# Performance work log

Measured on AMD Instinct MI355X. Metric: run time of the kernel, lower is better.

## Reference

```python
import jax, jax.numpy as jnp
import numpy as np
import itertools

# ---- static configuration (matches init_kwargs) ----
LS = [0, 1, 2, 3]            # spherical harmonic degrees, parity (-1)^l
MUL = 128                    # channel multiplicity of hklm / output
N_EDGES = 16384
DIMS = [2 * l + 1 for l in LS]
Y_DIM = sum(DIMS)                        # 16
H_DIM = sum(d * MUL for d in DIMS)       # 2048
Y_OFF = np.cumsum([0] + DIMS).tolist()
H_OFF = np.cumsum([0] + [d * MUL for d in DIMS]).tolist()

# ---- real-basis O(3) Clebsch-Gordan coefficients (numpy, setup-time) ----
def _su2_generators(l):
    m = np.arange(-l, l + 1)
    Lz = np.diag(m).astype(np.complex128)
    vals = np.sqrt(l * (l + 1) - m[:-1] * (m[:-1] + 1))
    Lp = np.zeros((2 * l + 1, 2 * l + 1), np.complex128)
    Lp[np.arange(1, 2 * l + 1), np.arange(2 * l)] = vals
    Lm = Lp.T.copy()
    return (Lp + Lm) / 2.0, (Lp - Lm) / 2.0j, Lz

def _c2r(l):
    # unitary change of basis: complex SH -> real SH
    d = 2 * l + 1
    U = np.zeros((d, d), np.complex128)
    U[l, l] = 1.0
    s2 = 1.0 / np.sqrt(2.0)
    for m in range(1, l + 1):
        U[l + m, l + m] = (-1) ** m * s2
        U[l + m, l - m] = s2
        U[l - m, l + m] = -1j * (-1) ** m * s2
        U[l - m, l - m] = 1j * s2
    return U

def _real_generators(l):
    U = _c2r(l)
    return [np.real(-1j * (U @ L @ U.conj().T)) for L in _su2_generators(l)]

def _cg(l1, l2, l3):
    # invariant tensor = null space of the summed infinitesimal rotation action
    G1, G2, G3 = _real_generators(l1), _real_generators(l2), _real_generators(l3)
    d1, d2, d3 = 2 * l1 + 1, 2 * l2 + 1, 2 * l3 + 1
    I1, I2, I3 = np.eye(d1), np.eye(d2), np.eye(d3)
    rows = []
    for k in range(3):
        rows.append(np.kron(np.kron(G1[k], I2), I3)
                    + np.kron(np.kron(I1, G2[k]), I3)
                    + np.kron(np.kron(I1, I2), G3[k]))
    K = np.concatenate(rows, axis=0)
    _, s, Vt = np.linalg.svd(K)
    c = Vt[-1].reshape(d1, d2, d3)
    c = c / np.linalg.norm(c)
    c = c * np.sign(c.reshape(-1)[np.argmax(np.abs(c))])  # deterministic sign
    return c

PATHS = []
_CG_LIST = []
for (i1, l1), (i2, l2), (i3, l3) in itertools.product(enumerate(LS), enumerate(LS), enumerate(LS)):
    # triangle inequality + O3 parity selection rule ((-1)^l parities)
    if abs(l1 - l2) <= l3 <= l1 + l2 and (l1 + l2 + l3) % 2 == 0:
        PATHS.append((i1, i2, i3))
        _CG_LIST.append(_cg(l1, l2, l3))
N_PATHS = len(PATHS)                    # 23
W_DIM = N_PATHS * MUL                   # 2944
CG_OFF = np.cumsum([0] + [c.size for c in _CG_LIST]).tolist()
CGC_NP = np.concatenate([c.reshape(-1) for c in _CG_LIST]).astype(np.float32)


def setup_inputs() -> dict:
    key = jax.random.key(0)
    k1, k2, k3 = jax.random.split(key, 3)
    return {
        "Ylm": jax.random.normal(k1, (N_EDGES, Y_DIM), jnp.float32),
        "hklm": jax.random.normal(k2, (N_EDGES, H_DIM), jnp.float32),
        "weight": jax.random.normal(k3, (N_EDGES, W_DIM), jnp.float32),
        "CGC": jnp.asarray(CGC_NP),   # registered buffer in the torch module
    }


def reference(Ylm, hklm, weight, CGC):
    # segmented tensor product 'abcu,a,bu,cu' with per-path weight fused in:
    # out[n, c, u] += sum_{a,b} CG_p[a,b,c] * w_p[n,u] * Y[n,a] * h[n,b,u]
    N = Ylm.shape[0]
    out = jnp.zeros((N, H_DIM), Ylm.dtype)
    for p, (i1, i2, i3) in enumerate(PATHS):
        d1, d2, d3 = DIMS[i1], DIMS[i2], DIMS[i3]
        cg = CGC[CG_OFF[p]:CG_OFF[p + 1]].reshape(d1, d2, d3)
        y = Ylm[:, Y_OFF[i1]:Y_OFF[i1] + d1]
        h = hklm[:, H_OFF[i2]:H_OFF[i2] + d2 * MUL].reshape(N, d2, MUL)
        w = weight[:, p * MUL:(p + 1) * MUL]
        z = jnp.einsum('abc,na,nbu->ncu', cg, y, h) * w[:, None, :]
        out = out.at[:, H_OFF[i3]:H_OFF[i3] + d3 * MUL].add(z.reshape(N, d3 * MUL))
    return out
```

## Files before the change

### kernel.cpp

```cpp
#include <hip/hip_runtime.h>


#define BS 256
#define GSZ 32
#define EPB 8
#define YD 16
#define HD 2048
#define WD 2944
#define NROW 99

#define FOR_PATHS(X) \
  X(0, 0,0,0,    0,  0) \
  X(1, 0,1,1,    1,  1) \
  X(2, 0,2,2,   10,  4) \
  X(3, 0,3,3,   35,  9) \
  X(4, 1,0,1,   84, 16) \
  X(5, 1,1,0,   93, 19) \
  X(6, 1,1,2,  102, 20) \
  X(7, 1,2,1,  147, 25) \
  X(8, 1,2,3,  192, 28) \
  X(9, 1,3,2,  297, 35) \
  X(10,2,0,2,  402, 40) \
  X(11,2,1,1,  427, 45) \
  X(12,2,1,3,  472, 48) \
  X(13,2,2,0,  577, 55) \
  X(14,2,2,2,  602, 56) \
  X(15,2,3,1,  727, 61) \
  X(16,2,3,3,  832, 64) \
  X(17,3,0,3, 1077, 71) \
  X(18,3,1,2, 1126, 78) \
  X(19,3,2,1, 1231, 83) \
  X(20,3,2,3, 1336, 86) \
  X(21,3,3,0, 1581, 93) \
  X(22,3,3,2, 1630, 94)

__host__ __device__ constexpr int coff(int l) {
  return l == 0 ? 0 : (l == 1 ? 1 : (l == 2 ? 4 : 9));
}

__global__ __launch_bounds__(BS, 2) void etp_kernel(
    const float* __restrict__ Y, const float* __restrict__ H,
    const float* __restrict__ W, const float* __restrict__ CG,
    float* __restrict__ O) {
  const int g = threadIdx.x >> 5;
  const int l = threadIdx.x & 31;
  const int n = blockIdx.x * EPB + g;

  __shared__ __align__(16) float Bsm[EPB][NROW * 8];
  __shared__ float ysm[EPB][YD];

  { const int t = threadIdx.x;
    if (t < EPB * YD) {
      const int e = t >> 4, c = t & 15;
      ysm[e][c] = Y[(size_t)(blockIdx.x * EPB + e) * YD + c];
    } }
  __syncthreads();

#define BUILD(P, L1, L2, L3, CGO, RO) { \
    constexpr int d1 = 2*(L1)+1, d2 = 2*(L2)+1, d3 = 2*(L3)+1; \
    _Pragma("unroll") \
    for (int it = 0; it < (d2 * d3 + GSZ - 1) / GSZ; ++it) { \
      const int idx = l + it * GSZ; \
      if (idx < d2 * d3) { \
        const int m3 = idx / d2, m2 = idx - m3 * d2; \
        float s = 0.f; \
        _Pragma("unroll") \
        for (int a = 0; a < d1; ++a) \
          s += CG[(CGO) + (a * d2 + m2) * d3 + m3] * ysm[g][coff(L1) + a]; \
        Bsm[g][((RO) + m3) * 8 + m2] = s; \
      } } }
  FOR_PATHS(BUILD)
#undef BUILD
  __syncthreads();

  const float4* __restrict__ Hp = (const float4*)(H + (size_t)n * HD);
  const float4* __restrict__ Wp = (const float4*)(W + (size_t)n * WD);
  float4* __restrict__ Op = (float4*)(O + (size_t)n * HD);

  float4 h[YD];
#pragma unroll
  for (int c = 0; c < YD; ++c) h[c] = Hp[c * GSZ + l];
#pragma unroll
  for (int c = 0; c < YD; ++c)
    asm volatile("" : "+v"(h[c].x), "+v"(h[c].y), "+v"(h[c].z), "+v"(h[c].w));

  float4 acc[YD];
#pragma unroll
  for (int c = 0; c < YD; ++c) acc[c] = make_float4(0.f, 0.f, 0.f, 0.f);

#define DOPATH(P, L1, L2, L3, CGO, RO) { \
    constexpr int d2 = 2*(L2)+1, d3 = 2*(L3)+1; \
    const float4 wv = Wp[(P) * GSZ + l]; \
    _Pragma("unroll") \
    for (int m3 = 0; m3 < d3; ++m3) { \
      const float4* row = (const float4*)&Bsm[g][((RO) + m3) * 8]; \
      float br[8]; \
      *(float4*)&br[0] = row[0]; \
      if (d2 > 4) *(float4*)&br[4] = row[1]; \
      float4 s = make_float4(0.f, 0.f, 0.f, 0.f); \
      _Pragma("unroll") \
      for (int m2 = 0; m2 < d2; ++m2) { \
        const float b = br[m2]; \
        const float4 hv = h[coff(L2) + m2]; \
        s.x += b * hv.x; s.y += b * hv.y; s.z += b * hv.z; s.w += b * hv.w; \
      } \
      float4& A = acc[coff(L3) + m3]; \
      A.x += s.x * wv.x; A.y += s.y * wv.y; A.z += s.z * wv.z; A.w += s.w * wv.w; \
    } }
  FOR_PATHS(DOPATH)
#undef DOPATH

#pragma unroll
  for (int c = 0; c < YD; ++c) Op[c * GSZ + l] = acc[c];
}

extern "C" void kernel_launch(void* const* d_in, const int* in_sizes, int n_in,
                              void* d_out, int out_size, void* d_ws, size_t ws_size,
                              hipStream_t stream) {
  const float* Y  = (const float*)d_in[0];
  const float* H  = (const float*)d_in[1];
  const float* W  = (const float*)d_in[2];
  const float* CG = (const float*)d_in[3];
  float* O = (float*)d_out;

  const int n_edges = in_sizes[0] / YD;
  etp_kernel<<<n_edges / EPB, BS, 0, stream>>>(Y, H, W, CG, O);
}
```

Baseline: 115.0 us.

## Preload all path weights, use ext_vector float4 math, nontemporal output stores

```diff
diff --git a/kernel.cpp b/kernel.cpp
--- a/kernel.cpp
+++ b/kernel.cpp
@@ -7,7 +7,10 @@
 #define YD 16
 #define HD 2048
 #define WD 2944
+#define NP 23
 #define NROW 99
+
+typedef float f4 __attribute__((ext_vector_type(4)));
 
 #define FOR_PATHS(X) \
   X(0, 0,0,0,    0,  0) \
@@ -38,7 +41,9 @@
   return l == 0 ? 0 : (l == 1 ? 1 : (l == 2 ? 4 : 9));
 }
 
-__global__ __launch_bounds__(BS, 2) void etp_kernel(
+__global__ __launch_bounds__(BS)
+__attribute__((amdgpu_waves_per_eu(2, 2)))
+void etp_kernel(
     const float* __restrict__ Y, const float* __restrict__ H,
     const float* __restrict__ W, const float* __restrict__ CG,
     float* __restrict__ O) {
@@ -73,45 +78,41 @@
 #undef BUILD
   __syncthreads();
 
-  const float4* __restrict__ Hp = (const float4*)(H + (size_t)n * HD);
-  const float4* __restrict__ Wp = (const float4*)(W + (size_t)n * WD);
-  float4* __restrict__ Op = (float4*)(O + (size_t)n * HD);
+  const f4* __restrict__ Hp = (const f4*)(H + (size_t)n * HD);
+  const f4* __restrict__ Wp = (const f4*)(W + (size_t)n * WD);
+  f4* __restrict__ Op = (f4*)(O + (size_t)n * HD);
 
-  float4 h[YD];
+  f4 h[YD];
 #pragma unroll
   for (int c = 0; c < YD; ++c) h[c] = Hp[c * GSZ + l];
+  f4 wv[NP];
 #pragma unroll
-  for (int c = 0; c < YD; ++c)
-    asm volatile("" : "+v"(h[c].x), "+v"(h[c].y), "+v"(h[c].z), "+v"(h[c].w));
+  for (int p = 0; p < NP; ++p) wv[p] = Wp[p * GSZ + l];
 
-  float4 acc[YD];
+  f4 acc[YD];
 #pragma unroll
-  for (int c = 0; c < YD; ++c) acc[c] = make_float4(0.f, 0.f, 0.f, 0.f);
+  for (int c = 0; c < YD; ++c) acc[c] = (f4)0.f;
 
 #define DOPATH(P, L1, L2, L3, CGO, RO) { \
     constexpr int d2 = 2*(L2)+1, d3 = 2*(L3)+1; \
-    const float4 wv = Wp[(P) * GSZ + l]; \
     _Pragma("unroll") \
     for (int m3 = 0; m3 < d3; ++m3) { \
-      const float4* row = (const float4*)&Bsm[g][((RO) + m3) * 8]; \
+      const f4* row = (const f4*)&Bsm[g][((RO) + m3) * 8]; \
       float br[8]; \
-      *(float4*)&br[0] = row[0]; \
-      if (d2 > 4) *(float4*)&br[4] = row[1]; \
-      float4 s = make_float4(0.f, 0.f, 0.f, 0.f); \
+      *(f4*)&br[0] = row[0]; \
+      if (d2 > 4) *(f4*)&br[4] = row[1]; \
+      f4 s = (f4)0.f; \
       _Pragma("unroll") \
-      for (int m2 = 0; m2 < d2; ++m2) { \
-        const float b = br[m2]; \
-        const float4 hv = h[coff(L2) + m2]; \
-        s.x += b * hv.x; s.y += b * hv.y; s.z += b * hv.z; s.w += b * hv.w; \
-      } \
-      float4& A = acc[coff(L3) + m3]; \
-      A.x += s.x * wv.x; A.y += s.y * wv.y; A.z += s.z * wv.z; A.w += s.w * wv.w; \
+      for (int m2 = 0; m2 < d2; ++m2) \
+        s += br[m2] * h[coff(L2) + m2]; \
+      acc[coff(L3) + m3] += s * wv[P]; \
     } }
   FOR_PATHS(DOPATH)
 #undef DOPATH
 
 #pragma unroll
-  for (int c = 0; c < YD; ++c) Op[c * GSZ + l] = acc[c];
+  for (int c = 0; c < YD; ++c)
+    __builtin_nontemporal_store(acc[c], &Op[c * GSZ + l]);
 }
 
 extern "C" void kernel_launch(void* const* d_in, const int* in_sizes, int n_in,
```

Measured after the change: 107.5 us. 1.07x faster.
